# Performance work log

Hardware: AMD Instinct MI355X
Metric: run time of the kernel (lower is better)

Reference implementation:

```python
import jax, jax.numpy as jnp
import numpy as np

EPS = 1e-15
MAX_TANH_ARG = 1.0 - 1e-5  # clamp for artanh domain, standard in Poincare-ball libs


def logmap0(x):
    # Poincare ball, c=1: logmap0(x) = artanh(||x||) * x / ||x||
    norm = jnp.linalg.norm(x, axis=-1, keepdims=True)
    norm_c = jnp.clip(norm, EPS, MAX_TANH_ARG)
    scale = jnp.arctanh(norm_c) / jnp.maximum(norm, EPS)
    return scale * x


def expmap0(v):
    # Poincare ball, c=1: expmap0(v) = tanh(||v||) * v / ||v||
    norm = jnp.linalg.norm(v, axis=-1, keepdims=True)
    scale = jnp.tanh(norm) / jnp.maximum(norm, EPS)
    return scale * v


def setup_inputs() -> dict:
    key = jax.random.key(0)
    k1, k2, k3, k4 = jax.random.split(key, 4)
    N, E, D_IN, D_OUT = 50000, 600000, 128, 128
    # points loosely inside/near the ball; logmap0 clamps the norm anyway
    x = jax.random.uniform(k1, (N, D_IN), dtype=jnp.float32)
    edge_index = jax.random.randint(k2, (2, E), 0, N, dtype=jnp.int32)
    W = jax.random.normal(k3, (D_OUT, D_IN), dtype=jnp.float32) / np.sqrt(D_IN)
    b = jax.random.normal(k4, (D_OUT,), dtype=jnp.float32) * 0.01
    return {"x": x, "edge_index": edge_index, "W": W, "b": b}


def reference(x, edge_index, W, b):
    num_nodes = x.shape[0]
    src, dst = edge_index[0], edge_index[1]

    x_tangent = logmap0(x)                       # [N, D_in]
    h = x_tangent @ W.T + b                      # [N, D_out]

    # symmetric degree count: each edge adds 1 to dst and 1 to src
    ones = jnp.ones(src.shape[0], dtype=jnp.float32)
    deg = (jax.ops.segment_sum(ones, dst, num_segments=num_nodes)
           + jax.ops.segment_sum(ones, src, num_segments=num_nodes))
    deg = jnp.maximum(deg, 1.0)
    dinv = deg ** -0.5                           # [N]

    # fused gather-scale-scatter across ALL feature dims at once
    msg = h[src] * (dinv[src] * dinv[dst])[:, None]   # [E, D_out]
    out = jax.ops.segment_sum(msg, dst, num_segments=num_nodes)  # [N, D_out]

    return expmap0(out)
```

## Files before the change

### kernel.cpp

```cpp
#include <hip/hip_runtime.h>
#include <math.h>

#define D 128
#define CAP 48
#define NS 32
#define HWPAD 12512
#define HBH (NS * 2)
#define HB (HBH * 2)
#define BKB 64

typedef __attribute__((ext_vector_type(8))) short short8;
typedef __attribute__((ext_vector_type(4))) float f32x4;

__device__ inline unsigned short f2bf(float f) {
  unsigned int u = __float_as_uint(f);
  u = (u + 0x7FFFu + ((u >> 16) & 1u)) >> 16;
  return (unsigned short)u;
}
__device__ inline float bf2f(unsigned int us) {
  return __uint_as_float(us << 16);
}

__global__ __launch_bounds__(256) void k_prep(
    const float* __restrict__ W, const int* __restrict__ src,
    const int* __restrict__ dst, unsigned int* __restrict__ e32,
    unsigned short* __restrict__ Wbf, unsigned int* __restrict__ cursor,
    unsigned int* __restrict__ part, unsigned char* __restrict__ rank, int N,
    int E, int fancy) {
  const int t = threadIdx.x;
  const int bid = blockIdx.x;

  if (bid < HB) {
    if (!fancy) return;
    __shared__ unsigned int lh[HWPAD];
    const int kind = bid >> 6;
    const int sb = bid & 63;
    const int s = sb >> 1, hf = sb & 1;
    const int W16 = (N + 1) >> 1;
    const int HW = (W16 + 1) >> 1;
    const unsigned int baseW = (unsigned)(hf * HW);
    for (int i = t; i < HWPAD; i += 256) lh[i] = 0u;
    __syncthreads();
    const int e0 = (int)((long long)s * E / NS);
    const int e1 = (int)((long long)(s + 1) * E / NS);
    if (kind == 0) {
      for (int e = e0 + t; e < e1; e += 256) {
        int n = dst[e];
        unsigned int wk = ((unsigned)n >> 1) - baseW;
        if (wk < (unsigned)HW) {
          int sh = (n & 1) << 4;
          unsigned int old = atomicAdd(&lh[wk], 1u << sh);
          unsigned int rk = (old >> sh) & 0xFFFFu;
          rank[e] = (unsigned char)(rk > 255u ? 255u : rk);
        }
      }
    } else {
      for (int e = e0 + t; e < e1; e += 256) {
        int n = src[e];
        unsigned int wk = ((unsigned)n >> 1) - baseW;
        if (wk < (unsigned)HW) atomicAdd(&lh[wk], 1u << ((n & 1) << 4));
      }
    }
    __syncthreads();
    uint4* po = (uint4*)(part + (size_t)(kind * HBH + sb) * HWPAD);
    const uint4* li = (const uint4*)lh;
    for (int i = t; i < HWPAD / 4; i += 256) po[i] = li[i];
    return;
  }

  int g = (bid - HB) * 256 + t;
  if (g < N) cursor[g] = 0u;
  if (fancy) {
    int e = g * 4;
    if (e + 3 < E) {
      int4 s4 = *(const int4*)(src + e);
      int4 d4 = *(const int4*)(dst + e);
      uint4 p;
      p.x = ((unsigned)d4.x << 16) | (unsigned)s4.x;
      p.y = ((unsigned)d4.y << 16) | (unsigned)s4.y;
      p.z = ((unsigned)d4.z << 16) | (unsigned)s4.z;
      p.w = ((unsigned)d4.w << 16) | (unsigned)s4.w;
      *(uint4*)(e32 + e) = p;
    } else if (e < E) {
      for (int k = e; k < E; ++k)
        e32[k] = ((unsigned)dst[k] << 16) | (unsigned)src[k];
    }
  }
  int i = g * 4;
  if (i < D * D) {
    float4 wv = *(const float4*)(W + i);
    int r = i >> 7, c = i & 127;
    int idx = ((c >> 3) << 10) + (r << 3) + (c & 7);
    *(ushort4*)(&Wbf[idx]) =
        make_ushort4(f2bf(wv.x), f2bf(wv.y), f2bf(wv.z), f2bf(wv.w));
  }
}

__global__ __launch_bounds__(256) void k_reduce(
    const unsigned int* __restrict__ part, float* __restrict__ dinv,
    unsigned int* __restrict__ cntv, unsigned short* __restrict__ pre, int N) {
  const int W16 = (N + 1) >> 1;
  const int HW = (W16 + 1) >> 1;
  int wd = blockIdx.x * 256 + threadIdx.x;
  if (wd >= W16) return;
  int hf = (wd >= HW);
  int lw = wd - hf * HW;
  int n0 = wd * 2;
  unsigned int run = 0, so = 0;
#pragma unroll
  for (int s = 0; s < NS; ++s) {
    unsigned short* pp = pre + (size_t)s * N + n0;
    pp[0] = (unsigned short)(run & 0xFFFFu);
    if (n0 + 1 < N) pp[1] = (unsigned short)(run >> 16);
    run += part[(size_t)(s * 2 + hf) * HWPAD + lw];
    so += part[(size_t)(HBH + s * 2 + hf) * HWPAD + lw];
  }
  unsigned int in0 = run & 0xFFFFu, in1 = run >> 16;
  cntv[n0] = in0;
  dinv[n0] = rsqrtf(fmaxf((float)(in0 + (so & 0xFFFFu)), 1.0f));
  if (n0 + 1 < N) {
    cntv[n0 + 1] = in1;
    dinv[n0 + 1] = rsqrtf(fmaxf((float)(in1 + (so >> 16)), 1.0f));
  }
}

__global__ __launch_bounds__(256) void k_main(
    const float* __restrict__ x, const unsigned short* __restrict__ Wbf,
    const float* __restrict__ bvec, const int* __restrict__ src,
    const int* __restrict__ dst, const unsigned int* __restrict__ e32,
    unsigned int* __restrict__ cursor, int* __restrict__ ebuf,
    const unsigned char* __restrict__ rank,
    const unsigned short* __restrict__ pre, unsigned short* __restrict__ h,
    int N, int E, int fancy) {
  const int t = threadIdx.x;
  const int bid = blockIdx.x;

  if (bid < BKB) {
    if (fancy) {
      const int s = bid >> 1;
      const int e0 = (int)((long long)s * E / NS);
      const int e1 = (int)((long long)(s + 1) * E / NS);
      const unsigned short* ps = pre + (size_t)s * N;
      for (int e = e0 + (bid & 1) * 256 + t; e < e1; e += 512) {
        unsigned int v = e32[e];
        int d_ = (int)(v >> 16);
        unsigned int slot = (unsigned int)ps[d_] + (unsigned int)rank[e];
        if (slot < CAP) ebuf[(size_t)d_ * CAP + slot] = (int)(v & 0xFFFFu);
      }
    } else {
      const int e0 = (int)((long long)bid * E / BKB);
      const int e1 = (int)((long long)(bid + 1) * E / BKB);
      for (int e = e0 + t; e < e1; e += 256) {
        int d_ = dst[e], s_ = src[e];
        unsigned int p = atomicAdd(&cursor[d_], 1u) & 0xFFFFu;
        if (p < CAP) ebuf[(size_t)d_ * CAP + p] = s_;
        atomicAdd(&cursor[s_], 0x10000u);
      }
    }
    return;
  }

  const int gb = bid - BKB;
  const int w = t >> 6;
  const int l = t & 63;
  const int lc = l & 15;
  const int q = l >> 4;
  const int r0 = gb * 64;
  const int grow = r0 + w * 16 + lc;
  const bool ok = grow < N;
  const float* xp = x + (size_t)grow * D + q * 8;

  short8 a[4];
  float ss = 0.0f;
#pragma unroll
  for (int kk = 0; kk < 4; ++kk) {
    float4 u = ok ? *(const float4*)(xp + kk * 32) : make_float4(0, 0, 0, 0);
    float4 v = ok ? *(const float4*)(xp + kk * 32 + 4) : make_float4(0, 0, 0, 0);
    ss += u.x * u.x + u.y * u.y + u.z * u.z + u.w * u.w;
    ss += v.x * v.x + v.y * v.y + v.z * v.z + v.w * v.w;
    short8 af;
    af[0] = (short)f2bf(u.x); af[1] = (short)f2bf(u.y);
    af[2] = (short)f2bf(u.z); af[3] = (short)f2bf(u.w);
    af[4] = (short)f2bf(v.x); af[5] = (short)f2bf(v.y);
    af[6] = (short)f2bf(v.z); af[7] = (short)f2bf(v.w);
    a[kk] = af;
  }
  ss += __shfl_xor(ss, 16, 64);
  ss += __shfl_xor(ss, 32, 64);
  float nrm = sqrtf(ss);
  float nc = fminf(fmaxf(nrm, 1e-15f), 1.0f - 1e-5f);
  float rs = atanhf(nc) / fmaxf(nrm, 1e-15f);

  f32x4 acc[8];
#pragma unroll
  for (int nt = 0; nt < 8; ++nt) acc[nt] = (f32x4){0.f, 0.f, 0.f, 0.f};

#pragma unroll
  for (int kk = 0; kk < 4; ++kk) {
#pragma unroll
    for (int nt = 0; nt < 8; ++nt) {
      short8 bf =
          *(const short8*)(Wbf + ((kk * 4 + q) << 10) + ((nt * 16 + lc) << 3));
      acc[nt] = __builtin_amdgcn_mfma_f32_16x16x32_bf16(a[kk], bf, acc[nt], 0, 0, 0);
    }
  }

  float rsl[4];
#pragma unroll
  for (int i = 0; i < 4; ++i) rsl[i] = __shfl(rs, q * 4 + i, 64);

#pragma unroll
  for (int nt = 0; nt < 8; ++nt) {
    int j = nt * 16 + lc;
    float bj = bvec[j];
#pragma unroll
    for (int i = 0; i < 4; ++i) {
      int gr = r0 + w * 16 + q * 4 + i;
      if (gr < N) h[(size_t)gr * D + j] = f2bf(rsl[i] * acc[nt][i] + bj);
    }
  }
}

__global__ __launch_bounds__(256) void k_gather(
    const unsigned short* __restrict__ h, const int* __restrict__ ebuf,
    const unsigned int* __restrict__ cursor, const float* __restrict__ dinv,
    const unsigned int* __restrict__ cntv, float* __restrict__ out, int N,
    int fancy) {
  int gid = blockIdx.x * 256 + threadIdx.x;
  int r = gid >> 5;
  int sub = threadIdx.x & 31;
  if (r >= N) return;

  int cnt;
  float di_d;
  if (fancy) {
    cnt = (int)cntv[r];
    di_d = dinv[r];
  } else {
    unsigned int cr = cursor[r];
    cnt = (int)(cr & 0xFFFFu);
    di_d = rsqrtf(fmaxf((float)((cr & 0xFFFFu) + (cr >> 16)), 1.0f));
  }
  if (cnt > CAP) cnt = CAP;
  const int* eb = ebuf + (size_t)r * CAP;

  int c1 = cnt < 32 ? cnt : 32;
  int s_a = (sub < c1) ? eb[sub] : 0;
  float dv_a = 0.0f;
  if (sub < c1) {
    if (fancy) dv_a = dinv[s_a];
    else {
      unsigned int vs = cursor[s_a];
      dv_a = rsqrtf(fmaxf((float)((vs & 0xFFFFu) + (vs >> 16)), 1.0f));
    }
  }
  int s_b = (sub + 32 < cnt) ? eb[32 + sub] : 0;
  float dv_b = 0.0f;
  if (sub + 32 < cnt) {
    if (fancy) dv_b = dinv[s_b];
    else {
      unsigned int vs = cursor[s_b];
      dv_b = rsqrtf(fmaxf((float)((vs & 0xFFFFu) + (vs >> 16)), 1.0f));
    }
  }

  float a0 = 0.f, a1 = 0.f, a2 = 0.f, a3 = 0.f;
  for (int i = 0; i < c1; i += 8) {
    uint2 pv[8];
    float wj[8];
#pragma unroll
    for (int j = 0; j < 8; ++j) {
      int s = __shfl(s_a, i + j, 32);
      wj[j] = __shfl(dv_a, i + j, 32);
      pv[j] = *(const uint2*)(h + (size_t)s * D + sub * 4);
    }
#pragma unroll
    for (int j = 0; j < 8; ++j) {
      a0 += wj[j] * bf2f(pv[j].x & 0xFFFFu);
      a1 += wj[j] * bf2f(pv[j].x >> 16);
      a2 += wj[j] * bf2f(pv[j].y & 0xFFFFu);
      a3 += wj[j] * bf2f(pv[j].y >> 16);
    }
  }
  for (int i = 0; i < cnt - 32; i += 8) {
    uint2 pv[8];
    float wj[8];
#pragma unroll
    for (int j = 0; j < 8; ++j) {
      int s = __shfl(s_b, i + j, 32);
      wj[j] = __shfl(dv_b, i + j, 32);
      pv[j] = *(const uint2*)(h + (size_t)s * D + sub * 4);
    }
#pragma unroll
    for (int j = 0; j < 8; ++j) {
      a0 += wj[j] * bf2f(pv[j].x & 0xFFFFu);
      a1 += wj[j] * bf2f(pv[j].x >> 16);
      a2 += wj[j] * bf2f(pv[j].y & 0xFFFFu);
      a3 += wj[j] * bf2f(pv[j].y >> 16);
    }
  }

  a0 *= di_d; a1 *= di_d; a2 *= di_d; a3 *= di_d;

  float sN = a0 * a0 + a1 * a1 + a2 * a2 + a3 * a3;
#pragma unroll
  for (int off = 16; off > 0; off >>= 1) sN += __shfl_down(sN, off, 32);
  sN = __shfl(sN, 0, 32);
  float n = sqrtf(sN);
  float sc = tanhf(n) / fmaxf(n, 1e-15f);

  float4* op = (float4*)(out + (size_t)r * D);
  op[sub] = make_float4(a0 * sc, a1 * sc, a2 * sc, a3 * sc);
}

extern "C" void kernel_launch(void* const* d_in, const int* in_sizes, int n_in,
                              void* d_out, int out_size, void* d_ws, size_t ws_size,
                              hipStream_t stream) {
  const float* x = (const float*)d_in[0];
  const int* ei = (const int*)d_in[1];
  const float* W = (const float*)d_in[2];
  const float* b = (const float*)d_in[3];
  float* out = (float*)d_out;

  const int N = in_sizes[0] / D;
  const int E = in_sizes[1] / 2;
  const int* src = ei;
  const int* dst = ei + E;

  size_t o_ebuf = ((size_t)N * D * 2 + 63) & ~(size_t)63;
  size_t o_cur = (o_ebuf + (size_t)N * CAP * 4 + 63) & ~(size_t)63;
  size_t o_dinv = (o_cur + (size_t)N * 4 + 63) & ~(size_t)63;
  size_t o_cnt = (o_dinv + (size_t)N * 4 + 63) & ~(size_t)63;
  size_t o_wbf = (o_cnt + (size_t)N * 4 + 63) & ~(size_t)63;
  size_t o_e32 = (o_wbf + 32768 + 63) & ~(size_t)63;
  size_t o_part = (o_e32 + (size_t)E * 4 + 63) & ~(size_t)63;
  size_t o_pre = (o_part + (size_t)HB * HWPAD * 4 + 63) & ~(size_t)63;
  size_t o_rank = (o_pre + (size_t)NS * N * 2 + 63) & ~(size_t)63;
  size_t need = o_rank + (size_t)E;

  unsigned short* h = (unsigned short*)d_ws;
  int* ebuf = (int*)((char*)d_ws + o_ebuf);
  unsigned int* cursor = (unsigned int*)((char*)d_ws + o_cur);
  float* dinv = (float*)((char*)d_ws + o_dinv);
  unsigned int* cntv = (unsigned int*)((char*)d_ws + o_cnt);
  unsigned short* Wbf = (unsigned short*)((char*)d_ws + o_wbf);
  unsigned int* e32 = (unsigned int*)((char*)d_ws + o_e32);
  unsigned int* part = (unsigned int*)((char*)d_ws + o_part);
  unsigned short* pre = (unsigned short*)((char*)d_ws + o_pre);
  unsigned char* rank = (unsigned char*)((char*)d_ws + o_rank);

  const int W16 = (N + 1) >> 1;
  const int HW = (W16 + 1) >> 1;
  const int fancy = (HW <= HWPAD) && (N <= 65535) && (ws_size >= need);

  int PBn = (N + 255) / 256;
  int PBe = ((E + 3) / 4 + 255) / 256;
  int PB = PBn > 16 ? PBn : 16;
  if (fancy && PBe > PB) PB = PBe;
  k_prep<<<HB + PB, 256, 0, stream>>>(W, src, dst, e32, Wbf, cursor, part, rank,
                                      N, E, fancy);

  if (fancy)
    k_reduce<<<(W16 + 255) / 256, 256, 0, stream>>>(part, dinv, cntv, pre, N);

  const int NBG = (N + 63) / 64;
  k_main<<<BKB + NBG, 256, 0, stream>>>(x, Wbf, b, src, dst, e32, cursor, ebuf,
                                        rank, pre, h, N, E, fancy);
  k_gather<<<(int)(((long long)N * 32 + 255) / 256), 256, 0, stream>>>(
      h, ebuf, cursor, dinv, cntv, out, N, fancy);
}
```

Measured before the change: 171.7 us.

## Use 8-bit per-node histograms with more edge slices and node-major prefix layout

After: 148.8 us. 1.15x faster.

```diff
diff --git a/kernel.cpp b/kernel.cpp
--- a/kernel.cpp
+++ b/kernel.cpp
@@ -3,11 +3,11 @@
 
 #define D 128
 #define CAP 48
-#define NS 32
-#define HWPAD 12512
-#define HBH (NS * 2)
-#define HB (HBH * 2)
-#define BKB 64
+#define NS 64
+#define HB2 (NS * 2)
+#define HBT (HB2 * 2)
+#define HLDS 28672
+#define BKB 128
 
 typedef __attribute__((ext_vector_type(8))) short short8;
 typedef __attribute__((ext_vector_type(4))) float f32x4;
@@ -23,69 +23,50 @@
 
 __global__ __launch_bounds__(256) void k_prep(
     const float* __restrict__ W, const int* __restrict__ src,
-    const int* __restrict__ dst, unsigned int* __restrict__ e32,
-    unsigned short* __restrict__ Wbf, unsigned int* __restrict__ cursor,
-    unsigned int* __restrict__ part, unsigned char* __restrict__ rank, int N,
-    int E, int fancy) {
+    const int* __restrict__ dst, unsigned short* __restrict__ Wbf,
+    unsigned int* __restrict__ cursor, unsigned char* __restrict__ part8,
+    unsigned char* __restrict__ rank, int N, int E, int HP, int fancy) {
   const int t = threadIdx.x;
   const int bid = blockIdx.x;
 
-  if (bid < HB) {
+  if (bid < HBT) {
     if (!fancy) return;
-    __shared__ unsigned int lh[HWPAD];
-    const int kind = bid >> 6;
-    const int sb = bid & 63;
+    __shared__ unsigned int lh[HLDS / 4];
+    const int kind = bid >> 7;
+    const int sb = bid & 127;
     const int s = sb >> 1, hf = sb & 1;
-    const int W16 = (N + 1) >> 1;
-    const int HW = (W16 + 1) >> 1;
-    const unsigned int baseW = (unsigned)(hf * HW);
-    for (int i = t; i < HWPAD; i += 256) lh[i] = 0u;
+    const int H = (N + 1) >> 1;
+    const int G16 = (H + 15) >> 4;
+    for (int i = t; i < G16; i += 256) ((uint4*)lh)[i] = make_uint4(0, 0, 0, 0);
     __syncthreads();
     const int e0 = (int)((long long)s * E / NS);
     const int e1 = (int)((long long)(s + 1) * E / NS);
+    const int hbase = hf * H;
     if (kind == 0) {
       for (int e = e0 + t; e < e1; e += 256) {
         int n = dst[e];
-        unsigned int wk = ((unsigned)n >> 1) - baseW;
-        if (wk < (unsigned)HW) {
-          int sh = (n & 1) << 4;
-          unsigned int old = atomicAdd(&lh[wk], 1u << sh);
-          unsigned int rk = (old >> sh) & 0xFFFFu;
-          rank[e] = (unsigned char)(rk > 255u ? 255u : rk);
+        unsigned int lw = (unsigned)(n - hbase);
+        if (lw < (unsigned)H) {
+          int sh = (lw & 3) << 3;
+          unsigned int old = atomicAdd(&lh[lw >> 2], 1u << sh);
+          rank[e] = (unsigned char)((old >> sh) & 0xFFu);
         }
       }
     } else {
       for (int e = e0 + t; e < e1; e += 256) {
         int n = src[e];
-        unsigned int wk = ((unsigned)n >> 1) - baseW;
-        if (wk < (unsigned)HW) atomicAdd(&lh[wk], 1u << ((n & 1) << 4));
+        unsigned int lw = (unsigned)(n - hbase);
+        if (lw < (unsigned)H) atomicAdd(&lh[lw >> 2], 1u << ((lw & 3) << 3));
       }
     }
     __syncthreads();
-    uint4* po = (uint4*)(part + (size_t)(kind * HBH + sb) * HWPAD);
-    const uint4* li = (const uint4*)lh;
-    for (int i = t; i < HWPAD / 4; i += 256) po[i] = li[i];
+    uint4* po = (uint4*)(part8 + (size_t)bid * HP);
+    for (int i = t; i < G16; i += 256) po[i] = ((const uint4*)lh)[i];
     return;
   }
 
-  int g = (bid - HB) * 256 + t;
+  int g = (bid - HBT) * 256 + t;
   if (g < N) cursor[g] = 0u;
-  if (fancy) {
-    int e = g * 4;
-    if (e + 3 < E) {
-      int4 s4 = *(const int4*)(src + e);
-      int4 d4 = *(const int4*)(dst + e);
-      uint4 p;
-      p.x = ((unsigned)d4.x << 16) | (unsigned)s4.x;
-      p.y = ((unsigned)d4.y << 16) | (unsigned)s4.y;
-      p.z = ((unsigned)d4.z << 16) | (unsigned)s4.z;
-      p.w = ((unsigned)d4.w << 16) | (unsigned)s4.w;
-      *(uint4*)(e32 + e) = p;
-    } else if (e < E) {
-      for (int k = e; k < E; ++k)
-        e32[k] = ((unsigned)dst[k] << 16) | (unsigned)src[k];
-    }
-  }
   int i = g * 4;
   if (i < D * D) {
     float4 wv = *(const float4*)(W + i);
@@ -97,39 +78,40 @@
 }
 
 __global__ __launch_bounds__(256) void k_reduce(
-    const unsigned int* __restrict__ part, float* __restrict__ dinv,
-    unsigned int* __restrict__ cntv, unsigned short* __restrict__ pre, int N) {
-  const int W16 = (N + 1) >> 1;
-  const int HW = (W16 + 1) >> 1;
-  int wd = blockIdx.x * 256 + threadIdx.x;
-  if (wd >= W16) return;
-  int hf = (wd >= HW);
-  int lw = wd - hf * HW;
-  int n0 = wd * 2;
+    const unsigned char* __restrict__ part8, float* __restrict__ dinv,
+    unsigned int* __restrict__ cntv, unsigned short* __restrict__ pre, int N,
+    int HP) {
+  int n = blockIdx.x * 256 + threadIdx.x;
+  if (n >= N) return;
+  const int H = (N + 1) >> 1;
+  int hf = (n >= H);
+  int lw = n - hf * H;
   unsigned int run = 0, so = 0;
+  unsigned int pk[NS / 2];
 #pragma unroll
   for (int s = 0; s < NS; ++s) {
-    unsigned short* pp = pre + (size_t)s * N + n0;
-    pp[0] = (unsigned short)(run & 0xFFFFu);
-    if (n0 + 1 < N) pp[1] = (unsigned short)(run >> 16);
-    run += part[(size_t)(s * 2 + hf) * HWPAD + lw];
-    so += part[(size_t)(HBH + s * 2 + hf) * HWPAD + lw];
-  }
-  unsigned int in0 = run & 0xFFFFu, in1 = run >> 16;
-  cntv[n0] = in0;
-  dinv[n0] = rsqrtf(fmaxf((float)(in0 + (so & 0xFFFFu)), 1.0f));
-  if (n0 + 1 < N) {
-    cntv[n0 + 1] = in1;
-    dinv[n0 + 1] = rsqrtf(fmaxf((float)(in1 + (so >> 16)), 1.0f));
-  }
+    unsigned int cin = part8[(size_t)(s * 2 + hf) * HP + lw];
+    unsigned int cot = part8[(size_t)(HB2 + s * 2 + hf) * HP + lw];
+    if (s & 1)
+      pk[s >> 1] |= run << 16;
+    else
+      pk[s >> 1] = run;
+    run += cin;
+    so += cot;
+  }
+  uint4* pp = (uint4*)(pre + (size_t)n * NS);
+#pragma unroll
+  for (int i = 0; i < NS / 8; ++i)
+    pp[i] = make_uint4(pk[i * 4], pk[i * 4 + 1], pk[i * 4 + 2], pk[i * 4 + 3]);
+  cntv[n] = run;
+  dinv[n] = rsqrtf(fmaxf((float)(run + so), 1.0f));
 }
 
 __global__ __launch_bounds__(256) void k_main(
     const float* __restrict__ x, const unsigned short* __restrict__ Wbf,
     const float* __restrict__ bvec, const int* __restrict__ src,
-    const int* __restrict__ dst, const unsigned int* __restrict__ e32,
-    unsigned int* __restrict__ cursor, int* __restrict__ ebuf,
-    const unsigned char* __restrict__ rank,
+    const int* __restrict__ dst, unsigned int* __restrict__ cursor,
+    int* __restrict__ ebuf, const unsigned char* __restrict__ rank,
     const unsigned short* __restrict__ pre, unsigned short* __restrict__ h,
     int N, int E, int fancy) {
   const int t = threadIdx.x;
@@ -140,12 +122,11 @@
       const int s = bid >> 1;
       const int e0 = (int)((long long)s * E / NS);
       const int e1 = (int)((long long)(s + 1) * E / NS);
-      const unsigned short* ps = pre + (size_t)s * N;
       for (int e = e0 + (bid & 1) * 256 + t; e < e1; e += 512) {
-        unsigned int v = e32[e];
-        int d_ = (int)(v >> 16);
-        unsigned int slot = (unsigned int)ps[d_] + (unsigned int)rank[e];
-        if (slot < CAP) ebuf[(size_t)d_ * CAP + slot] = (int)(v & 0xFFFFu);
+        int d_ = dst[e];
+        unsigned int slot =
+            (unsigned int)pre[(size_t)d_ * NS + s] + (unsigned int)rank[e];
+        if (slot < CAP) ebuf[(size_t)d_ * CAP + slot] = src[e];
       }
     } else {
       const int e0 = (int)((long long)bid * E / BKB);
@@ -327,15 +308,17 @@
   const int* src = ei;
   const int* dst = ei + E;
 
+  const int H = (N + 1) >> 1;
+  const int HP = (H + 255) & ~255;
+
   size_t o_ebuf = ((size_t)N * D * 2 + 63) & ~(size_t)63;
   size_t o_cur = (o_ebuf + (size_t)N * CAP * 4 + 63) & ~(size_t)63;
   size_t o_dinv = (o_cur + (size_t)N * 4 + 63) & ~(size_t)63;
   size_t o_cnt = (o_dinv + (size_t)N * 4 + 63) & ~(size_t)63;
   size_t o_wbf = (o_cnt + (size_t)N * 4 + 63) & ~(size_t)63;
-  size_t o_e32 = (o_wbf + 32768 + 63) & ~(size_t)63;
-  size_t o_part = (o_e32 + (size_t)E * 4 + 63) & ~(size_t)63;
-  size_t o_pre = (o_part + (size_t)HB * HWPAD * 4 + 63) & ~(size_t)63;
-  size_t o_rank = (o_pre + (size_t)NS * N * 2 + 63) & ~(size_t)63;
+  size_t o_p8 = (o_wbf + 32768 + 255) & ~(size_t)255;
+  size_t o_pre = (o_p8 + (size_t)HBT * HP + 63) & ~(size_t)63;
+  size_t o_rank = (o_pre + (size_t)N * NS * 2 + 63) & ~(size_t)63;
   size_t need = o_rank + (size_t)E;
 
   unsigned short* h = (unsigned short*)d_ws;
@@ -344,28 +327,23 @@
   float* dinv = (float*)((char*)d_ws + o_dinv);
   unsigned int* cntv = (unsigned int*)((char*)d_ws + o_cnt);
   unsigned short* Wbf = (unsigned short*)((char*)d_ws + o_wbf);
-  unsigned int* e32 = (unsigned int*)((char*)d_ws + o_e32);
-  unsigned int* part = (unsigned int*)((char*)d_ws + o_part);
+  unsigned char* part8 = (unsigned char*)((char*)d_ws + o_p8);
   unsigned short* pre = (unsigned short*)((char*)d_ws + o_pre);
   unsigned char* rank = (unsigned char*)((char*)d_ws + o_rank);
 
-  const int W16 = (N + 1) >> 1;
-  const int HW = (W16 + 1) >> 1;
-  const int fancy = (HW <= HWPAD) && (N <= 65535) && (ws_size >= need);
+  const int fancy = (H <= HLDS) && (N <= 65535) && (ws_size >= need);
 
   int PBn = (N + 255) / 256;
-  int PBe = ((E + 3) / 4 + 255) / 256;
   int PB = PBn > 16 ? PBn : 16;
-  if (fancy && PBe > PB) PB = PBe;
-  k_prep<<<HB + PB, 256, 0, stream>>>(W, src, dst, e32, Wbf, cursor, part, rank,
-                                      N, E, fancy);
+  k_prep<<<HBT + PB, 256, 0, stream>>>(W, src, dst, Wbf, cursor, part8, rank, N,
+                                       E, HP, fancy);
 
   if (fancy)
-    k_reduce<<<(W16 + 255) / 256, 256, 0, stream>>>(part, dinv, cntv, pre, N);
+    k_reduce<<<(N + 255) / 256, 256, 0, stream>>>(part8, dinv, cntv, pre, N, HP);
 
   const int NBG = (N + 63) / 64;
-  k_main<<<BKB + NBG, 256, 0, stream>>>(x, Wbf, b, src, dst, e32, cursor, ebuf,
-                                        rank, pre, h, N, E, fancy);
+  k_main<<<BKB + NBG, 256, 0, stream>>>(x, Wbf, b, src, dst, cursor, ebuf, rank,
+                                        pre, h, N, E, fancy);
   k_gather<<<(int)(((long long)N * 32 + 255) / 256), 256, 0, stream>>>(
       h, ebuf, cursor, dinv, cntv, out, N, fancy);
 }
```
